# Performance work log

Hardware: AMD Instinct MI355X
Metric: run time of the kernel (lower is better)

## Reference

```python
import jax, jax.numpy as jnp
import numpy as np

LRELU_SLOPE = 0.2  # PyG GATConv default negative_slope
LN_EPS = 1e-5


def _layer_norm(x, g, b):
    mu = x.mean(-1, keepdims=True)
    var = x.var(-1, keepdims=True)
    return (x - mu) / jnp.sqrt(var + LN_EPS) * g + b


def _gat_conv(x, src, dst, W, a_src, a_dst, bias, heads, out_c, concat):
    # PyG GATConv (eval mode, self-loops already appended to src/dst).
    N = x.shape[0]
    h = (x @ W).reshape(N, heads, out_c)            # [N,H,C]
    e_src = (h * a_src).sum(-1)                     # [N,H]
    e_dst = (h * a_dst).sum(-1)                     # [N,H]
    e = jax.nn.leaky_relu(e_src[src] + e_dst[dst], LRELU_SLOPE)  # [E,H]
    # segment softmax over incoming edges of each dst node
    m = jax.ops.segment_max(e, dst, num_segments=N)
    m = jnp.where(jnp.isfinite(m), m, 0.0)
    w = jnp.exp(e - m[dst])
    denom = jax.ops.segment_sum(w, dst, num_segments=N)
    alpha = w / (denom[dst] + 1e-16)                # [E,H]
    out = jax.ops.segment_sum(h[src] * alpha[:, :, None], dst, num_segments=N)  # [N,H,C]
    out = out.reshape(N, heads * out_c) if concat else out.mean(1)
    return out + bias


def setup_inputs() -> dict:
    key = jax.random.key(0)
    ks = jax.random.split(key, 16)
    N, E, F0, Hd, H, G = 50000, 800000, 32, 32, 4, 512
    s = 0.1
    nrm = lambda k, shape: jax.random.normal(k, shape, jnp.float32) * s
    d = {}
    d['x'] = jax.random.normal(ks[0], (N, F0), jnp.float32)
    d['edge_index'] = jax.random.randint(ks[1], (2, E), 0, N)
    d['batch'] = jnp.sort(jax.random.randint(ks[2], (N,), 0, G))
    d['num_graphs'] = G
    # layer 1: F0 -> (Hd, H heads, concat)
    d['W1'] = nrm(ks[3], (F0, H * Hd)); d['as1'] = nrm(ks[4], (H, Hd)); d['ad1'] = nrm(ks[5], (H, Hd))
    d['b1'] = jnp.zeros((H * Hd,)); d['g1'] = jnp.ones((H * Hd,)); d['be1'] = jnp.zeros((H * Hd,))
    # layer 2: H*Hd -> (Hd, H heads, concat)
    d['W2'] = nrm(ks[6], (H * Hd, H * Hd)); d['as2'] = nrm(ks[7], (H, Hd)); d['ad2'] = nrm(ks[8], (H, Hd))
    d['b2'] = jnp.zeros((H * Hd,)); d['g2'] = jnp.ones((H * Hd,)); d['be2'] = jnp.zeros((H * Hd,))
    # layer 3: H*Hd -> (Hd, 1 head, mean)
    d['W3'] = nrm(ks[9], (H * Hd, Hd)); d['as3'] = nrm(ks[10], (1, Hd)); d['ad3'] = nrm(ks[11], (1, Hd))
    d['b3'] = jnp.zeros((Hd,)); d['g3'] = jnp.ones((Hd,)); d['be3'] = jnp.zeros((Hd,))
    # classifier MLP: 2*Hd -> Hd -> Hd//2 -> 1 (torch Linear [out,in])
    d['cW1'] = nrm(ks[12], (Hd, 2 * Hd)); d['cb1'] = jnp.zeros((Hd,))
    d['cW2'] = nrm(ks[13], (Hd // 2, Hd)); d['cb2'] = jnp.zeros((Hd // 2,))
    d['cW3'] = nrm(ks[14], (1, Hd // 2)); d['cb3'] = jnp.zeros((1,))
    return d


def reference(x, edge_index, batch, num_graphs,
              W1, as1, ad1, b1, g1, be1,
              W2, as2, ad2, b2, g2, be2,
              W3, as3, ad3, b3, g3, be3,
              cW1, cb1, cW2, cb2, cW3, cb3):
    N = x.shape[0]
    loop = jnp.arange(N)
    src = jnp.concatenate([edge_index[0], loop])
    dst = jnp.concatenate([edge_index[1], loop])
    h = jax.nn.elu(_layer_norm(_gat_conv(x, src, dst, W1, as1, ad1, b1, 4, 32, True), g1, be1))
    h = jax.nn.elu(_layer_norm(_gat_conv(h, src, dst, W2, as2, ad2, b2, 4, 32, True), g2, be2))
    h = jax.nn.elu(_layer_norm(_gat_conv(h, src, dst, W3, as3, ad3, b3, 1, 32, False), g3, be3))
    cnt = jax.ops.segment_sum(jnp.ones((N,), h.dtype), batch, num_segments=num_graphs)
    x_mean = jax.ops.segment_sum(h, batch, num_segments=num_graphs) / jnp.maximum(cnt, 1.0)[:, None]
    x_max = jax.ops.segment_max(h, batch, num_segments=num_graphs)
    f = jnp.concatenate([x_mean, x_max], axis=1)        # [G, 64]
    f = jax.nn.relu(f @ cW1.T + cb1)
    f = jax.nn.relu(f @ cW2.T + cb2)
    return (f @ cW3.T + cb3).squeeze(-1)                 # [G]
```

## Files before the change

### kernel.cpp

```cpp
#include <hip/hip_runtime.h>
#include <hip/hip_fp16.h>
#include <math.h>

#define CDIV(a, b) (((a) + (b) - 1) / (b))
#define SCAN_BS 1024
#define NBUK 512
#define ATILE 4096

typedef _Float16 f16x8 __attribute__((ext_vector_type(8)));
typedef float f32x4 __attribute__((ext_vector_type(4)));

__device__ __forceinline__ unsigned encf(float v) {
    unsigned u = __float_as_uint(v);
    return (u & 0x80000000u) ? ~u : (u | 0x80000000u);
}
__device__ __forceinline__ float decf(unsigned k) {
    unsigned u = (k & 0x80000000u) ? (k ^ 0x80000000u) : ~k;
    return __uint_as_float(u);
}

__device__ __forceinline__ float lrelu(float v) {
    return v > 0.f ? v : 0.2f * v;
}

__global__ __launch_bounds__(256) void gemm_kernel(
    const float* __restrict__ X, const float* __restrict__ W,
    float* __restrict__ Y, int M, int K, int Nout) {
    int idx = blockIdx.x * blockDim.x + threadIdx.x;
    if (idx >= M * Nout) return;
    int row = idx / Nout;
    int col = idx - row * Nout;
    const float* xr = X + (size_t)row * K;
    const float* wc = W + col;
    float acc = 0.f;
    for (int k = 0; k < K; k += 4) {
        float4 xv = *(const float4*)(xr + k);
        acc += xv.x * wc[(size_t)(k + 0) * Nout];
        acc += xv.y * wc[(size_t)(k + 1) * Nout];
        acc += xv.z * wc[(size_t)(k + 2) * Nout];
        acc += xv.w * wc[(size_t)(k + 3) * Nout];
    }
    Y[idx] = acc;
}

__device__ __forceinline__ void wprep_one(const float* __restrict__ W,
                                          __half* __restrict__ Whf, int K,
                                          int NOUT, int idx) {
    int NK = K / 32;
    int l = idx & 63, f = idx >> 6;
    int ks = f % NK, tt = f / NK;
    int quad = l >> 4, c15 = l & 15;
    _Float16 v[8];
#pragma unroll
    for (int j = 0; j < 8; ++j) {
        int k = ks * 32 + quad * 8 + j;
        int n = tt * 16 + c15;
        v[j] = (_Float16)W[(size_t)k * NOUT + n];
    }
    *(uint4*)(Whf + (size_t)idx * 8) = *(uint4*)v;
}

__device__ __forceinline__ f16x8 loadA(const float* p) {
    float4 lo = *(const float4*)p;
    float4 hi = *(const float4*)(p + 4);
    f16x8 a;
    a[0] = (_Float16)lo.x; a[1] = (_Float16)lo.y;
    a[2] = (_Float16)lo.z; a[3] = (_Float16)lo.w;
    a[4] = (_Float16)hi.x; a[5] = (_Float16)hi.y;
    a[6] = (_Float16)hi.z; a[7] = (_Float16)hi.w;
    return a;
}
__device__ __forceinline__ f16x8 loadA(const __half* p) {
    return *(const f16x8*)p;
}

template <int K, int NOUT, int HH, typename XT>
__global__ __launch_bounds__(256) void gemm_mfma_attn(
    const XT* __restrict__ X, const __half* __restrict__ Whf,
    __half* __restrict__ Y, const float* __restrict__ a_src,
    const float* __restrict__ a_dst, float* __restrict__ es,
    float* __restrict__ ed, int M) {
    constexpr int NK = K / 32, NT = NOUT / 16;
    static_assert(NT == 2 * HH, "32 channels per head assumed");
    int wave = threadIdx.x >> 6, lane = threadIdx.x & 63;
    int quad = lane >> 4, c15 = lane & 15;
    int row0 = (blockIdx.x * 4 + wave) * 16;
    if (row0 >= M) return;
    int arow = row0 + c15;
    if (arow >= M) arow = M - 1;
    const XT* xr = X + (size_t)arow * K + quad * 8;
    const f16x8* bp = (const f16x8*)Whf;
    f32x4 acc[NT];
#pragma unroll
    for (int t = 0; t < NT; ++t) {
        acc[t][0] = 0.f; acc[t][1] = 0.f; acc[t][2] = 0.f; acc[t][3] = 0.f;
    }
#pragma unroll
    for (int ks = 0; ks < NK; ++ks) {
        f16x8 a = loadA(xr + ks * 32);
#pragma unroll
        for (int t = 0; t < NT; ++t) {
            f16x8 b = bp[(t * NK + ks) * 64 + lane];
            acc[t] = __builtin_amdgcn_mfma_f32_16x16x32_f16(a, b, acc[t],
                                                            0, 0, 0);
        }
    }
#pragma unroll
    for (int r = 0; r < 4; ++r) {
        int row = row0 + quad * 4 + r;
        if (row < M) {
#pragma unroll
            for (int t = 0; t < NT; ++t)
                Y[(size_t)row * NOUT + t * 16 + c15] = (__half)acc[t][r];
        }
    }
    float asv[NT], adv[NT];
#pragma unroll
    for (int t = 0; t < NT; ++t) {
        asv[t] = a_src[t * 16 + c15];
        adv[t] = a_dst[t * 16 + c15];
    }
#pragma unroll
    for (int h = 0; h < HH; ++h) {
#pragma unroll
        for (int r = 0; r < 4; ++r) {
            float s = acc[2 * h][r] * asv[2 * h] +
                      acc[2 * h + 1][r] * asv[2 * h + 1];
            float dd = acc[2 * h][r] * adv[2 * h] +
                       acc[2 * h + 1][r] * adv[2 * h + 1];
#pragma unroll
            for (int off = 8; off >= 1; off >>= 1) {
                s += __shfl_xor(s, off);
                dd += __shfl_xor(dd, off);
            }
            int row = row0 + quad * 4 + r;
            if (row < M) {
                if (c15 == 0) es[row * HH + h] = s;
                if (c15 == 1) ed[row * HH + h] = dd;
            }
        }
    }
}

__global__ __launch_bounds__(256) void binA1_kernel(
    const int* __restrict__ ei, int E, int* __restrict__ ghist,
    int* __restrict__ pool0, int poolN, const float* __restrict__ W1,
    const float* __restrict__ W2, const float* __restrict__ W3,
    __half* __restrict__ wh1, __half* __restrict__ wh2,
    __half* __restrict__ wh3, int* __restrict__ rowptr, int N, int nhist) {
    __shared__ int lh[NBUK];
    int t = threadIdx.x;
    if (blockIdx.x >= nhist) {
        int idx = (blockIdx.x - nhist) * 256 + t;
        if (idx == 0) rowptr[N] = E + N;
        if (idx < 512) {
            wprep_one(W1, wh1, 32, 128, idx);
        } else if (idx < 2560) {
            wprep_one(W2, wh2, 128, 128, idx - 512);
        } else if (idx < 3072) {
            wprep_one(W3, wh3, 128, 32, idx - 2560);
        }
        return;
    }
    int gid = blockIdx.x * 256 + t;
    if (gid < poolN) pool0[gid] = 0;
    for (int i = t; i < NBUK; i += 256) lh[i] = 0;
    __syncthreads();
    int base = blockIdx.x * ATILE;
#pragma unroll 4
    for (int j = 0; j < ATILE / 256; ++j) {
        int idx = base + t + 256 * j;
        if (idx < E) atomicAdd(&lh[ei[E + idx] >> 7], 1);
    }
    __syncthreads();
    int* gh = ghist + (size_t)blockIdx.x * NBUK;
    for (int i = t; i < NBUK; i += 256) gh[i] = lh[i];
}

__global__ __launch_bounds__(64) void binA2a_kernel(
    int* __restrict__ ghist, int* __restrict__ tot, int nblk) {
    int b = blockIdx.x;
    int lane = threadIdx.x;
    int accb = 0;
    for (int chunk = 0; chunk < nblk; chunk += 64) {
        int i = chunk + lane;
        int v = (i < nblk) ? ghist[(size_t)i * NBUK + b] : 0;
        int s = v;
        for (int off = 1; off < 64; off <<= 1) {
            int tv = __shfl_up(s, off);
            if (lane >= off) s += tv;
        }
        if (i < nblk) ghist[(size_t)i * NBUK + b] = s - v + accb;
        accb += __shfl(s, 63);
    }
    if (lane == 0) tot[b] = accb;
}

__device__ __forceinline__ void bucketScan(const int* __restrict__ tot,
                                           int* __restrict__ sc, int t,
                                           int& a0, int& a1, int& excl) {
    a0 = tot[2 * t];
    a1 = tot[2 * t + 1];
    int pair = a0 + a1;
    sc[t] = pair;
    __syncthreads();
#pragma unroll
    for (int off = 1; off < 256; off <<= 1) {
        int v = (t >= off) ? sc[t - off] : 0;
        __syncthreads();
        sc[t] += v;
        __syncthreads();
    }
    excl = sc[t] - pair;
}

__global__ __launch_bounds__(256) void binA3_kernel(
    const int* __restrict__ ei, int E, const int* __restrict__ ghist,
    const int* __restrict__ tot, unsigned* __restrict__ ebuf) {
    __shared__ int lcur[NBUK];
    __shared__ int sc[256];
    int t = threadIdx.x;
    int a0, a1, excl;
    bucketScan(tot, sc, t, a0, a1, excl);
    const int* gh = ghist + (size_t)blockIdx.x * NBUK;
    lcur[2 * t] = gh[2 * t] + excl;
    lcur[2 * t + 1] = gh[2 * t + 1] + excl + a0;
    __syncthreads();
    int base = blockIdx.x * ATILE;
#pragma unroll 4
    for (int j = 0; j < ATILE / 256; ++j) {
        int idx = base + t + 256 * j;
        if (idx < E) {
            int s = ei[idx];
            int d = ei[E + idx];
            int pos = atomicAdd(&lcur[d >> 7], 1);
            ebuf[pos] = ((unsigned)d << 16) | (unsigned)s;
        }
    }
}

__global__ __launch_bounds__(256) void binB_kernel(
    const unsigned* __restrict__ ebuf, const int* __restrict__ tot,
    int* __restrict__ rowptr, int* __restrict__ csrc, int N) {
    __shared__ int cnt_[128];
    __shared__ int pre[128];
    __shared__ int lcur[128];
    __shared__ int sc[256];
    __shared__ int begS;
    int b = blockIdx.x;
    int t = threadIdx.x;
    int n0 = b << 7;
    int totb = tot[b];
    if (t < 128) cnt_[t] = 0;
    int a0, a1, excl;
    bucketScan(tot, sc, t, a0, a1, excl);
    if (t == (b >> 1)) begS = (b & 1) ? (excl + a0) : excl;
    __syncthreads();
    int beg = begS, end = begS + totb;
    for (int i = beg + t; i < end; i += 256)
        atomicAdd(&cnt_[(ebuf[i] >> 16) - n0], 1);
    __syncthreads();
    if (t < 128) pre[t] = (n0 + t < N) ? (cnt_[t] + 1) : 0;
    __syncthreads();
    for (int off = 1; off < 128; off <<= 1) {
        int v = 0;
        if (t < 128 && t >= off) v = pre[t - off];
        __syncthreads();
        if (t < 128) pre[t] += v;
        __syncthreads();
    }
    int cbase = beg + n0;
    if (t < 128 && n0 + t < N) {
        int ex = pre[t] - (cnt_[t] + 1);
        int rp = cbase + ex;
        rowptr[n0 + t] = rp;
        csrc[rp] = n0 + t;
        lcur[t] = rp + 1;
    }
    __syncthreads();
    for (int i = beg + t; i < end; i += 256) {
        unsigned e = ebuf[i];
        int d = (int)(e >> 16) - n0;
        int s = (int)(e & 0xFFFFu);
        int pos = atomicAdd(&lcur[d], 1);
        csrc[pos] = s;
    }
}

__global__ __launch_bounds__(256) void attn_kernel(
    const float* __restrict__ h, const float* __restrict__ a_src,
    const float* __restrict__ a_dst, float* __restrict__ es,
    float* __restrict__ ed, int N, int H, int C) {
    int idx = blockIdx.x * blockDim.x + threadIdx.x;
    if (idx >= N * H) return;
    int n = idx / H;
    int hh = idx - n * H;
    const float* hp = h + (size_t)n * H * C + (size_t)hh * C;
    const float* ap = a_src + hh * C;
    const float* bp = a_dst + hh * C;
    float s = 0.f, d = 0.f;
    for (int c = 0; c < C; c += 4) {
        float4 hv = *(const float4*)(hp + c);
        float4 av = *(const float4*)(ap + c);
        float4 bv = *(const float4*)(bp + c);
        s += hv.x * av.x + hv.y * av.y + hv.z * av.z + hv.w * av.w;
        d += hv.x * bv.x + hv.y * bv.y + hv.z * bv.z + hv.w * bv.w;
    }
    es[idx] = s;
    ed[idx] = d;
}

__global__ __launch_bounds__(256) void deg_kernel(const int* __restrict__ ei,
                                                  int E,
                                                  int* __restrict__ deg) {
    int e = blockIdx.x * blockDim.x + threadIdx.x;
    if (e >= E) return;
    atomicAdd(&deg[ei[E + e]], 1);
}

__global__ __launch_bounds__(SCAN_BS) void scan1_kernel(
    const int* __restrict__ deg, int* __restrict__ rowptr,
    int* __restrict__ bsum, int N) {
    __shared__ int tmp[SCAN_BS];
    int tid = threadIdx.x;
    int gid = blockIdx.x * SCAN_BS + tid;
    int v = (gid < N) ? (deg[gid] + 1) : 0;
    tmp[tid] = v;
    __syncthreads();
    for (int off = 1; off < SCAN_BS; off <<= 1) {
        int t = (tid >= off) ? tmp[tid - off] : 0;
        __syncthreads();
        tmp[tid] += t;
        __syncthreads();
    }
    if (gid < N) rowptr[gid] = tmp[tid] - v;
    if (tid == SCAN_BS - 1) bsum[blockIdx.x] = tmp[tid];
}

__global__ void scan2_kernel(int* __restrict__ bsum, int nb) {
    if (threadIdx.x == 0 && blockIdx.x == 0) {
        int acc = 0;
        for (int i = 0; i < nb; ++i) {
            int t = bsum[i];
            bsum[i] = acc;
            acc += t;
        }
    }
}

__global__ __launch_bounds__(SCAN_BS) void scan3_kernel(
    int* __restrict__ rowptr, int* __restrict__ cursor,
    int* __restrict__ csrc, const int* __restrict__ bsum, int N, int total) {
    int gid = blockIdx.x * SCAN_BS + threadIdx.x;
    if (gid < N) {
        int v = rowptr[gid] + bsum[blockIdx.x];
        rowptr[gid] = v;
        cursor[gid] = v + 1;
        csrc[v] = gid;
    }
    if (gid == 0) rowptr[N] = total;
}

__global__ __launch_bounds__(256) void scatter_kernel(
    const int* __restrict__ ei, int E, int* __restrict__ cursor,
    int* __restrict__ csrc) {
    int e = blockIdx.x * blockDim.x + threadIdx.x;
    if (e >= E) return;
    int s = ei[e];
    int d = ei[E + e];
    int pos = atomicAdd(&cursor[d], 1);
    csrc[pos] = s;
}

__global__ __launch_bounds__(256) void aggr_ln128_kernel(
    const int* __restrict__ rowptr, const int* __restrict__ csrc,
    const __half* __restrict__ h, const float* __restrict__ es,
    const float* __restrict__ ed, const float* __restrict__ bias,
    const float* __restrict__ gam, const float* __restrict__ bet,
    __half* __restrict__ outp, int N) {
    constexpr int D = 128, H = 4;
    int d = (blockIdx.x * blockDim.x + threadIdx.x) >> 4;
    int cl = threadIdx.x & 15;
    if (d >= N) return;
    int c = cl * 8;
    int hh = cl >> 2;
    float edv = ed[d * H + hh];
    float acc[8];
#pragma unroll
    for (int i = 0; i < 8; ++i) acc[i] = 0.f;
    float l = 0.f;
    int k = rowptr[d], end = rowptr[d + 1];
    for (; k + 8 <= end; k += 8) {
        int s[8];
#pragma unroll
        for (int j = 0; j < 8; ++j) s[j] = csrc[k + j];
        float e[8];
#pragma unroll
        for (int j = 0; j < 8; ++j) e[j] = es[s[j] * H + hh];
        uint4 u[8];
#pragma unroll
        for (int j = 0; j < 8; ++j)
            u[j] = *(const uint4*)(h + (size_t)s[j] * D + c);
#pragma unroll
        for (int j = 0; j < 8; ++j) {
            float w = __expf(lrelu(e[j] + edv));
            l += w;
            const __half2* hp = (const __half2*)&u[j];
#pragma unroll
            for (int i = 0; i < 4; ++i) {
                float2 f = __half22float2(hp[i]);
                acc[2 * i] += w * f.x;
                acc[2 * i + 1] += w * f.y;
            }
        }
    }
    for (; k + 4 <= end; k += 4) {
        int s[4];
#pragma unroll
        for (int j = 0; j < 4; ++j) s[j] = csrc[k + j];
        float e[4];
#pragma unroll
        for (int j = 0; j < 4; ++j) e[j] = es[s[j] * H + hh];
        uint4 u[4];
#pragma unroll
        for (int j = 0; j < 4; ++j)
            u[j] = *(const uint4*)(h + (size_t)s[j] * D + c);
#pragma unroll
        for (int j = 0; j < 4; ++j) {
            float w = __expf(lrelu(e[j] + edv));
            l += w;
            const __half2* hp = (const __half2*)&u[j];
#pragma unroll
            for (int i = 0; i < 4; ++i) {
                float2 f = __half22float2(hp[i]);
                acc[2 * i] += w * f.x;
                acc[2 * i + 1] += w * f.y;
            }
        }
    }
    for (; k < end; ++k) {
        int s = csrc[k];
        float w = __expf(lrelu(es[s * H + hh] + edv));
        uint4 u = *(const uint4*)(h + (size_t)s * D + c);
        l += w;
        const __half2* hp = (const __half2*)&u;
#pragma unroll
        for (int i = 0; i < 4; ++i) {
            float2 f = __half22float2(hp[i]);
            acc[2 * i] += w * f.x;
            acc[2 * i + 1] += w * f.y;
        }
    }
    float rl = 1.f / (l + 1e-16f);
    float4 b0 = *(const float4*)(bias + c);
    float4 b1 = *(const float4*)(bias + c + 4);
    float v[8];
    v[0] = acc[0] * rl + b0.x; v[1] = acc[1] * rl + b0.y;
    v[2] = acc[2] * rl + b0.z; v[3] = acc[3] * rl + b0.w;
    v[4] = acc[4] * rl + b1.x; v[5] = acc[5] * rl + b1.y;
    v[6] = acc[6] * rl + b1.z; v[7] = acc[7] * rl + b1.w;
    float sm = 0.f, ssum = 0.f;
#pragma unroll
    for (int i = 0; i < 8; ++i) { sm += v[i]; ssum += v[i] * v[i]; }
#pragma unroll
    for (int off = 1; off <= 8; off <<= 1) {
        sm += __shfl_xor(sm, off);
        ssum += __shfl_xor(ssum, off);
    }
    float mean = sm / D;
    float var = ssum / D - mean * mean;
    float rstd = rsqrtf(var + 1e-5f);
    float4 g0 = *(const float4*)(gam + c);
    float4 g1 = *(const float4*)(gam + c + 4);
    float4 t0 = *(const float4*)(bet + c);
    float4 t1 = *(const float4*)(bet + c + 4);
    float gv[8] = {g0.x, g0.y, g0.z, g0.w, g1.x, g1.y, g1.z, g1.w};
    float tv[8] = {t0.x, t0.y, t0.z, t0.w, t1.x, t1.y, t1.z, t1.w};
    __half2 p[4];
#pragma unroll
    for (int i = 0; i < 4; ++i) {
        float o0 = (v[2 * i] - mean) * rstd * gv[2 * i] + tv[2 * i];
        float o1 = (v[2 * i + 1] - mean) * rstd * gv[2 * i + 1] + tv[2 * i + 1];
        o0 = o0 > 0.f ? o0 : expm1f(o0);
        o1 = o1 > 0.f ? o1 : expm1f(o1);
        p[i] = __floats2half2_rn(o0, o1);
    }
    uint4 uo;
    uo.x = *(unsigned*)&p[0];
    uo.y = *(unsigned*)&p[1];
    uo.z = *(unsigned*)&p[2];
    uo.w = *(unsigned*)&p[3];
    *(uint4*)(outp + (size_t)d * D + c) = uo;
}

__global__ __launch_bounds__(256) void aggr_ln32_pool_kernel(
    const int* __restrict__ rowptr, const int* __restrict__ csrc,
    const __half* __restrict__ h, const float* __restrict__ es,
    const float* __restrict__ ed, const float* __restrict__ bias,
    const float* __restrict__ gam, const float* __restrict__ bet,
    const int* __restrict__ batch, float* __restrict__ psum,
    unsigned* __restrict__ pmax, float* __restrict__ cnt, int N) {
    constexpr int D = 32;
    __shared__ float lsum[2][32];
    __shared__ unsigned lmax[2][32];
    __shared__ float lcnt[2];
    __shared__ int g0s;
    int tid = threadIdx.x;
    int d = (blockIdx.x * 256 + tid) >> 3;
    int cl = tid & 7;
    int c = cl * 4;
    int dbase = blockIdx.x * 32;
    if (tid < 64) {
        lsum[tid >> 5][tid & 31] = 0.f;
        lmax[tid >> 5][tid & 31] = 0u;
    }
    if (tid < 2) lcnt[tid] = 0.f;
    if (tid == 0) g0s = batch[dbase < N ? dbase : (N - 1)];
    __syncthreads();
    int g0 = g0s;
    if (d < N) {
        float edv = ed[d];
        float acc[4] = {0.f, 0.f, 0.f, 0.f};
        float l = 0.f;
        int k = rowptr[d], end = rowptr[d + 1];
        for (; k + 8 <= end; k += 8) {
            int s[8];
#pragma unroll
            for (int j = 0; j < 8; ++j) s[j] = csrc[k + j];
            float e[8];
#pragma unroll
            for (int j = 0; j < 8; ++j) e[j] = es[s[j]];
            uint2 u[8];
#pragma unroll
            for (int j = 0; j < 8; ++j)
                u[j] = *(const uint2*)(h + (size_t)s[j] * D + c);
#pragma unroll
            for (int j = 0; j < 8; ++j) {
                float w = __expf(lrelu(e[j] + edv));
                l += w;
                float2 f0 = __half22float2(*(__half2*)&u[j].x);
                float2 f1 = __half22float2(*(__half2*)&u[j].y);
                acc[0] += w * f0.x; acc[1] += w * f0.y;
                acc[2] += w * f1.x; acc[3] += w * f1.y;
            }
        }
        for (; k + 4 <= end; k += 4) {
            int s[4];
#pragma unroll
            for (int j = 0; j < 4; ++j) s[j] = csrc[k + j];
            float e[4];
#pragma unroll
            for (int j = 0; j < 4; ++j) e[j] = es[s[j]];
            uint2 u[4];
#pragma unroll
            for (int j = 0; j < 4; ++j)
                u[j] = *(const uint2*)(h + (size_t)s[j] * D + c);
#pragma unroll
            for (int j = 0; j < 4; ++j) {
                float w = __expf(lrelu(e[j] + edv));
                l += w;
                float2 f0 = __half22float2(*(__half2*)&u[j].x);
                float2 f1 = __half22float2(*(__half2*)&u[j].y);
                acc[0] += w * f0.x; acc[1] += w * f0.y;
                acc[2] += w * f1.x; acc[3] += w * f1.y;
            }
        }
        for (; k < end; ++k) {
            int s = csrc[k];
            float w = __expf(lrelu(es[s] + edv));
            uint2 u = *(const uint2*)(h + (size_t)s * D + c);
            l += w;
            float2 f0 = __half22float2(*(__half2*)&u.x);
            float2 f1 = __half22float2(*(__half2*)&u.y);
            acc[0] += w * f0.x; acc[1] += w * f0.y;
            acc[2] += w * f1.x; acc[3] += w * f1.y;
        }
        float rl = 1.f / (l + 1e-16f);
        float4 b4 = *(const float4*)(bias + c);
        float v0 = acc[0] * rl + b4.x;
        float v1 = acc[1] * rl + b4.y;
        float v2 = acc[2] * rl + b4.z;
        float v3 = acc[3] * rl + b4.w;
        float sm = v0 + v1 + v2 + v3;
        float ssum = v0 * v0 + v1 * v1 + v2 * v2 + v3 * v3;
#pragma unroll
        for (int off = 1; off <= 4; off <<= 1) {
            sm += __shfl_xor(sm, off);
            ssum += __shfl_xor(ssum, off);
        }
        float mean = sm / D;
        float var = ssum / D - mean * mean;
        float rstd = rsqrtf(var + 1e-5f);
        float4 g4 = *(const float4*)(gam + c);
        float4 t4 = *(const float4*)(bet + c);
        float o0 = (v0 - mean) * rstd * g4.x + t4.x;
        float o1 = (v1 - mean) * rstd * g4.y + t4.y;
        float o2 = (v2 - mean) * rstd * g4.z + t4.z;
        float o3 = (v3 - mean) * rstd * g4.w + t4.w;
        o0 = o0 > 0.f ? o0 : expm1f(o0);
        o1 = o1 > 0.f ? o1 : expm1f(o1);
        o2 = o2 > 0.f ? o2 : expm1f(o2);
        o3 = o3 > 0.f ? o3 : expm1f(o3);
        int g = batch[d];
        int goff = g - g0;
        if (goff >= 0 && goff < 2) {
            atomicAdd(&lsum[goff][c + 0], o0);
            atomicAdd(&lsum[goff][c + 1], o1);
            atomicAdd(&lsum[goff][c + 2], o2);
            atomicAdd(&lsum[goff][c + 3], o3);
            atomicMax(&lmax[goff][c + 0], encf(o0));
            atomicMax(&lmax[goff][c + 1], encf(o1));
            atomicMax(&lmax[goff][c + 2], encf(o2));
            atomicMax(&lmax[goff][c + 3], encf(o3));
            if (cl == 0) atomicAdd(&lcnt[goff], 1.0f);
        } else {
            atomicAdd(&psum[g * D + c + 0], o0);
            atomicAdd(&psum[g * D + c + 1], o1);
            atomicAdd(&psum[g * D + c + 2], o2);
            atomicAdd(&psum[g * D + c + 3], o3);
            atomicMax(&pmax[g * D + c + 0], encf(o0));
            atomicMax(&pmax[g * D + c + 1], encf(o1));
            atomicMax(&pmax[g * D + c + 2], encf(o2));
            atomicMax(&pmax[g * D + c + 3], encf(o3));
            if (cl == 0) atomicAdd(&cnt[g], 1.0f);
        }
    }
    __syncthreads();
    if (tid < 64) {
        int go = tid >> 5, cc = tid & 31;
        unsigned m = lmax[go][cc];
        if (m != 0u) {
            int gg = g0 + go;
            atomicAdd(&psum[gg * D + cc], lsum[go][cc]);
            atomicMax(&pmax[gg * D + cc], m);
            if (cc == 0) atomicAdd(&cnt[gg], lcnt[go]);
        }
    }
}

__global__ __launch_bounds__(256) void aggr_csr_kernel(
    const int* __restrict__ rowptr, const int* __restrict__ csrc,
    const float* __restrict__ h, const float* __restrict__ es,
    const float* __restrict__ ed, float* __restrict__ outp, int N, int H,
    int C) {
    int D = H * C;
    int wave = (blockIdx.x * blockDim.x + threadIdx.x) >> 6;
    int lane = threadIdx.x & 63;
    if (wave >= N) return;
    int d = wave;
    int c0 = lane, c1 = lane + 64;
    bool a0 = c0 < D, a1 = c1 < D;
    int h0 = a0 ? c0 / C : 0;
    int h1 = a1 ? c1 / C : 0;
    float edv0 = a0 ? ed[d * H + h0] : 0.f;
    float edv1 = a1 ? ed[d * H + h1] : 0.f;
    float m0 = -INFINITY, m1 = -INFINITY;
    float l0 = 0.f, l1 = 0.f, acc0 = 0.f, acc1 = 0.f;
    int beg = rowptr[d], end = rowptr[d + 1];
    for (int k = beg; k < end; ++k) {
        int s = csrc[k];
        const float* hp = h + (size_t)s * D;
        if (a0) {
            float v = lrelu(es[s * H + h0] + edv0);
            float nm = fmaxf(m0, v);
            float sc = __expf(m0 - nm);
            float w = __expf(v - nm);
            l0 = l0 * sc + w;
            acc0 = acc0 * sc + w * hp[c0];
            m0 = nm;
        }
        if (a1) {
            float v = lrelu(es[s * H + h1] + edv1);
            float nm = fmaxf(m1, v);
            float sc = __expf(m1 - nm);
            float w = __expf(v - nm);
            l1 = l1 * sc + w;
            acc1 = acc1 * sc + w * hp[c1];
            m1 = nm;
        }
    }
    if (a0) outp[(size_t)d * D + c0] = acc0 / (l0 + 1e-16f);
    if (a1) outp[(size_t)d * D + c1] = acc1 / (l1 + 1e-16f);
}

__global__ __launch_bounds__(64) void ln_elu_kernel(
    const float* __restrict__ in, const float* __restrict__ bias,
    const float* __restrict__ gam, const float* __restrict__ bet,
    float* __restrict__ outp, int D) {
    int n = blockIdx.x;
    int lane = threadIdx.x;
    int c0 = lane, c1 = lane + 64;
    bool a0 = c0 < D, a1 = c1 < D;
    float v0 = 0.f, v1 = 0.f;
    if (a0) v0 = in[(size_t)n * D + c0] + bias[c0];
    if (a1) v1 = in[(size_t)n * D + c1] + bias[c1];
    float s = v0 + v1;
    float ss = v0 * v0 + v1 * v1;
    for (int off = 32; off; off >>= 1) {
        s += __shfl_xor(s, off);
        ss += __shfl_xor(ss, off);
    }
    float mean = s / D;
    float var = ss / D - mean * mean;
    float rstd = rsqrtf(var + 1e-5f);
    if (a0) {
        float o = (v0 - mean) * rstd * gam[c0] + bet[c0];
        outp[(size_t)n * D + c0] = o > 0.f ? o : expm1f(o);
    }
    if (a1) {
        float o = (v1 - mean) * rstd * gam[c1] + bet[c1];
        outp[(size_t)n * D + c1] = o > 0.f ? o : expm1f(o);
    }
}

__global__ __launch_bounds__(256) void pool_kernel(
    const float* __restrict__ h, const int* __restrict__ batch, int N, int C,
    float* __restrict__ psum, unsigned* __restrict__ pmax,
    float* __restrict__ cnt) {
    int idx = blockIdx.x * blockDim.x + threadIdx.x;
    if (idx >= N * C) return;
    int n = idx / C;
    int c = idx - n * C;
    int g = batch[n];
    float v = h[(size_t)n * C + c];
    atomicAdd(&psum[g * C + c], v);
    atomicMax(&pmax[g * C + c], encf(v));
    if (c == 0) atomicAdd(&cnt[g], 1.0f);
}

__global__ __launch_bounds__(64) void mlp_kernel(
    const float* __restrict__ psum, const unsigned* __restrict__ pmax,
    const float* __restrict__ cnt, const float* __restrict__ cW1,
    const float* __restrict__ cb1, const float* __restrict__ cW2,
    const float* __restrict__ cb2, const float* __restrict__ cW3,
    const float* __restrict__ cb3, float* __restrict__ outp, int C) {
    __shared__ float f[64];
    __shared__ float t1[32];
    __shared__ float t2[16];
    int g = blockIdx.x;
    int t = threadIdx.x;
    float c = fmaxf(cnt[g], 1.0f);
    if (t < C) {
        f[t] = psum[g * C + t] / c;
    } else if (t < 2 * C) {
        unsigned k = pmax[g * C + (t - C)];
        f[t] = (k == 0u) ? -INFINITY : decf(k);
    }
    __syncthreads();
    if (t < 32) {
        float a = cb1[t];
        for (int i = 0; i < 64; ++i) a += f[i] * cW1[t * 64 + i];
        t1[t] = fmaxf(a, 0.f);
    }
    __syncthreads();
    if (t < 16) {
        float a = cb2[t];
        for (int i = 0; i < 32; ++i) a += t1[i] * cW2[t * 32 + i];
        t2[t] = fmaxf(a, 0.f);
    }
    __syncthreads();
    if (t == 0) {
        float a = cb3[0];
        for (int i = 0; i < 16; ++i) a += t2[i] * cW3[i];
        outp[g] = a;
    }
}

extern "C" void kernel_launch(void* const* d_in, const int* in_sizes, int n_in,
                              void* d_out, int out_size, void* d_ws,
                              size_t ws_size, hipStream_t stream) {
    const float* x = (const float*)d_in[0];
    const int* ei = (const int*)d_in[1];
    const int* batch = (const int*)d_in[2];
    const float* W1 = (const float*)d_in[4];
    const float* as1 = (const float*)d_in[5];
    const float* ad1 = (const float*)d_in[6];
    const float* b1 = (const float*)d_in[7];
    const float* g1 = (const float*)d_in[8];
    const float* be1 = (const float*)d_in[9];
    const float* W2 = (const float*)d_in[10];
    const float* as2 = (const float*)d_in[11];
    const float* ad2 = (const float*)d_in[12];
    const float* b2 = (const float*)d_in[13];
    const float* g2 = (const float*)d_in[14];
    const float* be2 = (const float*)d_in[15];
    const float* W3 = (const float*)d_in[16];
    const float* as3 = (const float*)d_in[17];
    const float* ad3 = (const float*)d_in[18];
    const float* b3 = (const float*)d_in[19];
    const float* g3 = (const float*)d_in[20];
    const float* be3 = (const float*)d_in[21];
    const float* cW1 = (const float*)d_in[22];
    const float* cb1 = (const float*)d_in[23];
    const float* cW2 = (const float*)d_in[24];
    const float* cb2 = (const float*)d_in[25];
    const float* cW3 = (const float*)d_in[26];
    const float* cb3 = (const float*)d_in[27];

    const int N = in_sizes[2];
    const int E = in_sizes[1] / 2;
    const int F0 = in_sizes[0] / N;
    const int Hd = in_sizes[19];
    const int H = in_sizes[5] / Hd;
    const int D = H * Hd;
    const int H3 = in_sizes[17] / Hd;
    const int G = out_size;
    const int EN = E + N;
    const bool shapes_ok = (F0 == 32 && Hd == 32 && H == 4 && D == 128 &&
                            H3 == 1 && N <= 65536);

    char* w = (char*)d_ws;
    size_t off = 0;
    auto carve = [&](size_t bytes) -> void* {
        void* p = w + off;
        off = (off + bytes + 255) & ~(size_t)255;
        return p;
    };
    float* Q = (float*)carve((size_t)N * D * 4);
    __half* Qh = (__half*)Q;
    float* R = (float*)carve((size_t)N * D * 4);
    float* P = (float*)carve((size_t)N * D * 4);
    __half* Ph = (__half*)P;
    float* es = (float*)carve((size_t)N * H * 4);
    float* ed = (float*)carve((size_t)N * H * 4);
    int* rowptr = (int*)carve((size_t)(N + 1) * 4);
    int* cursor = (int*)carve((size_t)N * 4);
    int* csrc = (int*)carve((size_t)EN * 4);
    int* bsum = (int*)carve((size_t)CDIV(N, SCAN_BS) * 4);
    const int nblkA = CDIV(E, ATILE);
    int* ghist = (int*)carve((size_t)nblkA * NBUK * 4);
    int* tot = (int*)carve((size_t)NBUK * 4);
    unsigned* ebuf = (unsigned*)carve((size_t)E * 4);
    __half* wh1 = (__half*)carve((size_t)8 * 1 * 64 * 8 * 2);
    __half* wh2 = (__half*)carve((size_t)8 * 4 * 64 * 8 * 2);
    __half* wh3 = (__half*)carve((size_t)2 * 4 * 64 * 8 * 2);
    float* psum = (float*)carve((size_t)G * Hd * 4);
    unsigned* pmax = (unsigned*)carve((size_t)G * Hd * 4);
    float* cnt = (float*)carve((size_t)G * 4);
    (void)ws_size;
    (void)n_in;

    const int BLK = 256;
    const int nb = CDIV(N, SCAN_BS);
    const int poolInts = G * Hd * 2 + G;

    if (shapes_ok) {
        binA1_kernel<<<nblkA + 12, 256, 0, stream>>>(
            ei, E, ghist, (int*)psum, poolInts, W1, W2, W3, wh1, wh2, wh3,
            rowptr, N, nblkA);
        binA2a_kernel<<<NBUK, 64, 0, stream>>>(ghist, tot, nblkA);
        binA3_kernel<<<nblkA, 256, 0, stream>>>(ei, E, ghist, tot, ebuf);
        binB_kernel<<<CDIV(N, 128), 256, 0, stream>>>(ebuf, tot, rowptr,
                                                      csrc, N);
        gemm_mfma_attn<32, 128, 4, float><<<CDIV(N, 64), 256, 0, stream>>>(
            x, wh1, Qh, as1, ad1, es, ed, N);
        aggr_ln128_kernel<<<CDIV(N, 16), 256, 0, stream>>>(
            rowptr, csrc, Qh, es, ed, b1, g1, be1, Ph, N);
        gemm_mfma_attn<128, 128, 4, __half><<<CDIV(N, 64), 256, 0, stream>>>(
            Ph, wh2, Qh, as2, ad2, es, ed, N);
        aggr_ln128_kernel<<<CDIV(N, 16), 256, 0, stream>>>(
            rowptr, csrc, Qh, es, ed, b2, g2, be2, Ph, N);
        gemm_mfma_attn<128, 32, 1, __half><<<CDIV(N, 64), 256, 0, stream>>>(
            Ph, wh3, Qh, as3, ad3, es, ed, N);
        aggr_ln32_pool_kernel<<<CDIV(N, 32), 256, 0, stream>>>(
            rowptr, csrc, Qh, es, ed, b3, g3, be3, batch, psum, pmax, cnt, N);
    } else {
        hipMemsetAsync(psum, 0, (size_t)G * Hd * 4, stream);
        hipMemsetAsync(pmax, 0, (size_t)G * Hd * 4, stream);
        hipMemsetAsync(cnt, 0, (size_t)G * 4, stream);
        hipMemsetAsync(cursor, 0, (size_t)N * 4, stream);
        deg_kernel<<<CDIV(E, BLK), BLK, 0, stream>>>(ei, E, cursor);
        scan1_kernel<<<nb, SCAN_BS, 0, stream>>>(cursor, rowptr, bsum, N);
        scan2_kernel<<<1, 64, 0, stream>>>(bsum, nb);
        scan3_kernel<<<nb, SCAN_BS, 0, stream>>>(rowptr, cursor, csrc, bsum, N, EN);
        scatter_kernel<<<CDIV(E, BLK), BLK, 0, stream>>>(ei, E, cursor, csrc);
        gemm_kernel<<<CDIV(N * D, BLK), BLK, 0, stream>>>(x, W1, Q, N, F0, D);
        attn_kernel<<<CDIV(N * H, BLK), BLK, 0, stream>>>(Q, as1, ad1, es, ed, N, H, Hd);
        aggr_csr_kernel<<<CDIV(N, 4), BLK, 0, stream>>>(rowptr, csrc, Q, es, ed, R, N, H, Hd);
        ln_elu_kernel<<<N, 64, 0, stream>>>(R, b1, g1, be1, P, D);
        gemm_kernel<<<CDIV(N * D, BLK), BLK, 0, stream>>>(P, W2, Q, N, D, D);
        attn_kernel<<<CDIV(N * H, BLK), BLK, 0, stream>>>(Q, as2, ad2, es, ed, N, H, Hd);
        aggr_csr_kernel<<<CDIV(N, 4), BLK, 0, stream>>>(rowptr, csrc, Q, es, ed, R, N, H, Hd);
        ln_elu_kernel<<<N, 64, 0, stream>>>(R, b2, g2, be2, P, D);
        gemm_kernel<<<CDIV(N * Hd, BLK), BLK, 0, stream>>>(P, W3, Q, N, D, Hd);
        attn_kernel<<<CDIV(N * H3, BLK), BLK, 0, stream>>>(Q, as3, ad3, es, ed, N, H3, Hd);
        aggr_csr_kernel<<<CDIV(N, 4), BLK, 0, stream>>>(rowptr, csrc, Q, es, ed, R, N, H3, Hd);
        ln_elu_kernel<<<N, 64, 0, stream>>>(R, b3, g3, be3, P, Hd);
        pool_kernel<<<CDIV(N * Hd, BLK), BLK, 0, stream>>>(P, batch, N, Hd, psum, pmax, cnt);
    }

    mlp_kernel<<<G, 64, 0, stream>>>(psum, pmax, cnt, cW1, cb1, cW2, cb2, cW3,
                                     cb3, (float*)d_out, Hd);
}
```

Measured before the change: 284.0 us.

## Fuse layer-1 GEMM into histogram kernel with per-block LDS weight prep

Moves the first-layer MFMA GEMM plus attention-score computation into the initial edge-histogram kernel as extra blocks. Each GEMM block converts W1 to fp16 fragments in shared memory, so the global wh1 buffer and one kernel launch are gone. The GEMM then runs alongside the histogram and weight-prep work instead of after binning. The cost is 8KB more LDS in every block of the combined kernel, which may lower histogram-block occupancy, and each GEMM block repeats the W1 conversion.

```diff
diff --git a/kernel.cpp b/kernel.cpp
--- a/kernel.cpp
+++ b/kernel.cpp
@@ -60,6 +60,23 @@
     *(uint4*)(Whf + (size_t)idx * 8) = *(uint4*)v;
 }
 
+__device__ __forceinline__ void wprep_one_lds(const float* __restrict__ W,
+                                              __half* Whf, int K, int NOUT,
+                                              int idx) {
+    int NK = K / 32;
+    int l = idx & 63, f = idx >> 6;
+    int ks = f % NK, tt = f / NK;
+    int quad = l >> 4, c15 = l & 15;
+    _Float16 v[8];
+#pragma unroll
+    for (int j = 0; j < 8; ++j) {
+        int k = ks * 32 + quad * 8 + j;
+        int n = tt * 16 + c15;
+        v[j] = (_Float16)W[(size_t)k * NOUT + n];
+    }
+    *(uint4*)(Whf + (size_t)idx * 8) = *(uint4*)v;
+}
+
 __device__ __forceinline__ f16x8 loadA(const float* p) {
     float4 lo = *(const float4*)p;
     float4 hi = *(const float4*)(p + 4);
@@ -74,22 +91,20 @@
     return *(const f16x8*)p;
 }
 
-template <int K, int NOUT, int HH, typename XT>
-__global__ __launch_bounds__(256) void gemm_mfma_attn(
-    const XT* __restrict__ X, const __half* __restrict__ Whf,
-    __half* __restrict__ Y, const float* __restrict__ a_src,
-    const float* __restrict__ a_dst, float* __restrict__ es,
-    float* __restrict__ ed, int M) {
+template <int K, int NOUT, int HH, typename XT, typename BP>
+__device__ __forceinline__ void gemm_attn_body(
+    const XT* __restrict__ X, const BP* bp, __half* __restrict__ Y,
+    const float* __restrict__ a_src, const float* __restrict__ a_dst,
+    float* __restrict__ es, float* __restrict__ ed, int M, int blk) {
     constexpr int NK = K / 32, NT = NOUT / 16;
     static_assert(NT == 2 * HH, "32 channels per head assumed");
     int wave = threadIdx.x >> 6, lane = threadIdx.x & 63;
     int quad = lane >> 4, c15 = lane & 15;
-    int row0 = (blockIdx.x * 4 + wave) * 16;
+    int row0 = (blk * 4 + wave) * 16;
     if (row0 >= M) return;
     int arow = row0 + c15;
     if (arow >= M) arow = M - 1;
     const XT* xr = X + (size_t)arow * K + quad * 8;
-    const f16x8* bp = (const f16x8*)Whf;
     f32x4 acc[NT];
 #pragma unroll
     for (int t = 0; t < NT; ++t) {
@@ -100,7 +115,7 @@
         f16x8 a = loadA(xr + ks * 32);
 #pragma unroll
         for (int t = 0; t < NT; ++t) {
-            f16x8 b = bp[(t * NK + ks) * 64 + lane];
+            f16x8 b = *(const f16x8*)&bp[((t * NK + ks) * 64 + lane) * 8];
             acc[t] = __builtin_amdgcn_mfma_f32_16x16x32_f16(a, b, acc[t],
                                                             0, 0, 0);
         }
@@ -142,23 +157,43 @@
     }
 }
 
+template <int K, int NOUT, int HH, typename XT>
+__global__ __launch_bounds__(256) void gemm_mfma_attn(
+    const XT* __restrict__ X, const __half* __restrict__ Whf,
+    __half* __restrict__ Y, const float* __restrict__ a_src,
+    const float* __restrict__ a_dst, float* __restrict__ es,
+    float* __restrict__ ed, int M) {
+    gemm_attn_body<K, NOUT, HH>(X, Whf, Y, a_src, a_dst, es, ed, M,
+                                blockIdx.x);
+}
+
 __global__ __launch_bounds__(256) void binA1_kernel(
     const int* __restrict__ ei, int E, int* __restrict__ ghist,
     int* __restrict__ pool0, int poolN, const float* __restrict__ W1,
     const float* __restrict__ W2, const float* __restrict__ W3,
-    __half* __restrict__ wh1, __half* __restrict__ wh2,
-    __half* __restrict__ wh3, int* __restrict__ rowptr, int N, int nhist) {
+    __half* __restrict__ wh2, __half* __restrict__ wh3,
+    int* __restrict__ rowptr, int N, int nhist, int nwp,
+    const float* __restrict__ x, __half* __restrict__ Qh,
+    const float* __restrict__ as1, const float* __restrict__ ad1,
+    float* __restrict__ es, float* __restrict__ ed) {
     __shared__ int lh[NBUK];
+    __shared__ __half wlds[512 * 8];
     int t = threadIdx.x;
+    if (blockIdx.x >= nhist + nwp) {
+        for (int i = t; i < 512; i += 256)
+            wprep_one_lds(W1, wlds, 32, 128, i);
+        __syncthreads();
+        gemm_attn_body<32, 128, 4>(x, wlds, Qh, as1, ad1, es, ed, N,
+                                   blockIdx.x - nhist - nwp);
+        return;
+    }
     if (blockIdx.x >= nhist) {
         int idx = (blockIdx.x - nhist) * 256 + t;
         if (idx == 0) rowptr[N] = E + N;
-        if (idx < 512) {
-            wprep_one(W1, wh1, 32, 128, idx);
+        if (idx < 2048) {
+            wprep_one(W2, wh2, 128, 128, idx);
         } else if (idx < 2560) {
-            wprep_one(W2, wh2, 128, 128, idx - 512);
-        } else if (idx < 3072) {
-            wprep_one(W3, wh3, 128, 32, idx - 2560);
+            wprep_one(W3, wh3, 128, 32, idx - 2048);
         }
         return;
     }
@@ -831,7 +866,6 @@
     int* ghist = (int*)carve((size_t)nblkA * NBUK * 4);
     int* tot = (int*)carve((size_t)NBUK * 4);
     unsigned* ebuf = (unsigned*)carve((size_t)E * 4);
-    __half* wh1 = (__half*)carve((size_t)8 * 1 * 64 * 8 * 2);
     __half* wh2 = (__half*)carve((size_t)8 * 4 * 64 * 8 * 2);
     __half* wh3 = (__half*)carve((size_t)2 * 4 * 64 * 8 * 2);
     float* psum = (float*)carve((size_t)G * Hd * 4);
@@ -845,15 +879,15 @@
     const int poolInts = G * Hd * 2 + G;
 
     if (shapes_ok) {
-        binA1_kernel<<<nblkA + 12, 256, 0, stream>>>(
-            ei, E, ghist, (int*)psum, poolInts, W1, W2, W3, wh1, wh2, wh3,
-            rowptr, N, nblkA);
+        const int nwp = 10;
+        const int ngemm1 = CDIV(N, 64);
+        binA1_kernel<<<nblkA + nwp + ngemm1, 256, 0, stream>>>(
+            ei, E, ghist, (int*)psum, poolInts, W1, W2, W3, wh2, wh3,
+            rowptr, N, nblkA, nwp, x, Qh, as1, ad1, es, ed);
         binA2a_kernel<<<NBUK, 64, 0, stream>>>(ghist, tot, nblkA);
         binA3_kernel<<<nblkA, 256, 0, stream>>>(ei, E, ghist, tot, ebuf);
         binB_kernel<<<CDIV(N, 128), 256, 0, stream>>>(ebuf, tot, rowptr,
                                                       csrc, N);
-        gemm_mfma_attn<32, 128, 4, float><<<CDIV(N, 64), 256, 0, stream>>>(
-            x, wh1, Qh, as1, ad1, es, ed, N);
         aggr_ln128_kernel<<<CDIV(N, 16), 256, 0, stream>>>(
             rowptr, csrc, Qh, es, ed, b1, g1, be1, Ph, N);
         gemm_mfma_attn<128, 128, 4, __half><<<CDIV(N, 64), 256, 0, stream>>>(
```

Measured after the change: 273.1 us. -3.8%, faster.
